# Optimization experiments

Measured on AMD Instinct MI355X. Metric: run time of the kernel, lower is better.

Reference implementation:

```python
import math
import jax, jax.numpy as jnp
import numpy as np

EMB = 1024
HEADS = 16
HEAD_DIM = EMB // HEADS
FF = 4 * EMB
EPS = 1e-5


def gelu_tanh(x):
    c = math.sqrt(2.0 / math.pi)
    return 0.5 * x * (1.0 + jnp.tanh(c * (x + 0.044715 * x ** 3)))


def layernorm(x, scale, shift):
    mean = jnp.mean(x, axis=-1, keepdims=True)
    var = jnp.var(x, axis=-1, keepdims=True)
    return scale * (x - mean) / jnp.sqrt(var + EPS) + shift


def setup_inputs() -> dict:
    key = jax.random.key(0)
    ks = jax.random.split(key, 10)
    s = 0.02
    return {
        "x": jax.random.normal(ks[0], (2, 2048, EMB), dtype=jnp.float32),
        "Wq": jax.random.normal(ks[1], (EMB, EMB), dtype=jnp.float32) * s,
        "Wk": jax.random.normal(ks[2], (EMB, EMB), dtype=jnp.float32) * s,
        "Wv": jax.random.normal(ks[3], (EMB, EMB), dtype=jnp.float32) * s,
        "Wo": jax.random.normal(ks[4], (EMB, EMB), dtype=jnp.float32) * s,
        "bo": jnp.zeros((EMB,), dtype=jnp.float32),
        "W1": jax.random.normal(ks[5], (EMB, FF), dtype=jnp.float32) * s,
        "b1": jnp.zeros((FF,), dtype=jnp.float32),
        "W2": jax.random.normal(ks[6], (FF, EMB), dtype=jnp.float32) * s,
        "b2": jnp.zeros((EMB,), dtype=jnp.float32),
        "ln1_scale": jnp.ones((EMB,), dtype=jnp.float32),
        "ln1_shift": jnp.zeros((EMB,), dtype=jnp.float32),
        "ln2_scale": jnp.ones((EMB,), dtype=jnp.float32),
        "ln2_shift": jnp.zeros((EMB,), dtype=jnp.float32),
    }


def reference(x, Wq, Wk, Wv, Wo, bo, W1, b1, W2, b2,
              ln1_scale, ln1_shift, ln2_scale, ln2_shift):
    B, S, D = x.shape
    # --- pre-LN causal MHA ---
    h = layernorm(x, ln1_scale, ln1_shift)
    q = (h @ Wq).reshape(B, S, HEADS, HEAD_DIM).transpose(0, 2, 1, 3)  # [B,H,S,d]
    k = (h @ Wk).reshape(B, S, HEADS, HEAD_DIM).transpose(0, 2, 1, 3)
    v = (h @ Wv).reshape(B, S, HEADS, HEAD_DIM).transpose(0, 2, 1, 3)
    scores = jnp.einsum("bhqd,bhkd->bhqk", q, k)  # [B,H,S,S]
    causal = jnp.triu(jnp.ones((S, S), dtype=bool), k=1)
    scores = jnp.where(causal, -jnp.inf, scores)
    attn = jax.nn.softmax(scores / math.sqrt(HEAD_DIM), axis=-1)
    ctx = jnp.einsum("bhqk,bhkd->bhqd", attn, v)  # [B,H,S,d]
    ctx = ctx.transpose(0, 2, 1, 3).reshape(B, S, D)
    x = x + (ctx @ Wo + bo)
    # --- FFN ---
    h = layernorm(x, ln2_scale, ln2_shift)
    h = gelu_tanh(h @ W1 + b1) @ W2 + b2
    return x + h
```

## Files before the change

### kernel.cpp

```cpp
#include <hip/hip_runtime.h>
#include <hip/hip_bf16.h>
#include <math.h>

#define EMB 1024
#define HEADS 16
#define HEAD_DIM 64
#define FF_DIM 4096
#define SEQ 2048
#define BATCH 2
#define NTOK (BATCH * SEQ)
#define LN_EPS 1e-5f
#define QKV_N 3072
#define Q_PRESCALE 0.18033688011112042f

typedef __attribute__((ext_vector_type(8))) short s8v;
typedef __attribute__((ext_vector_type(4))) float f4v;

__device__ __forceinline__ unsigned short f2bf(float f) {
    union { __hip_bfloat16 h; unsigned short u; } cv;
    cv.h = __float2bfloat16(f);
    return cv.u;
}

__device__ __forceinline__ float fast_exp2(float x) {
#if __has_builtin(__builtin_amdgcn_exp2f)
    return __builtin_amdgcn_exp2f(x);
#else
    return exp2f(x);
#endif
}

__device__ __forceinline__ float gelu_f(float x) {
    const float c = 0.7978845608028654f;
    float x3 = x * x * x;
    return 0.5f * x * (1.0f + tanhf(c * (x + 0.044715f * x3)));
}

#define GLDS(gp, lp)                                                        \
    __builtin_amdgcn_global_load_lds(                                       \
        (const __attribute__((address_space(1))) void*)(gp),                \
        (__attribute__((address_space(3))) void*)(lp), 16, 0, 0)

#define BAR()   do { __builtin_amdgcn_s_barrier(); __builtin_amdgcn_sched_barrier(0); } while (0)
#define LGKM0() do { asm volatile("s_waitcnt lgkmcnt(0)" ::: "memory"); __builtin_amdgcn_sched_barrier(0); } while (0)
#define VMCNT(n) do { asm volatile("s_waitcnt vmcnt(" #n ")" ::: "memory"); __builtin_amdgcn_sched_barrier(0); } while (0)

__global__ __launch_bounds__(256) void ln_bf16_kernel(const float* __restrict__ x,
                                                      const float* __restrict__ scale,
                                                      const float* __restrict__ shift,
                                                      unsigned short* __restrict__ out) {
    int row = blockIdx.x;
    int tid = threadIdx.x;
    const float4 xv = ((const float4*)(x + (size_t)row * EMB))[tid];
    float s  = xv.x + xv.y + xv.z + xv.w;
    float ss = xv.x * xv.x + xv.y * xv.y + xv.z * xv.z + xv.w * xv.w;
    __shared__ float2 red[256];
    red[tid] = make_float2(s, ss);
    __syncthreads();
    for (int off = 128; off > 0; off >>= 1) {
        if (tid < off) {
            red[tid].x += red[tid + off].x;
            red[tid].y += red[tid + off].y;
        }
        __syncthreads();
    }
    float mean = red[0].x * (1.0f / EMB);
    float var  = red[0].y * (1.0f / EMB) - mean * mean;
    float rstd = rsqrtf(var + LN_EPS);
    float4 sc4 = ((const float4*)scale)[tid];
    float4 sh4 = ((const float4*)shift)[tid];
    ushort4 o;
    o.x = f2bf(sc4.x * (xv.x - mean) * rstd + sh4.x);
    o.y = f2bf(sc4.y * (xv.y - mean) * rstd + sh4.y);
    o.z = f2bf(sc4.z * (xv.z - mean) * rstd + sh4.z);
    o.w = f2bf(sc4.w * (xv.w - mean) * rstd + sh4.w);
    *(ushort4*)(out + (size_t)row * EMB + tid * 4) = o;
}

__device__ __forceinline__ void tconv_tile(const float* __restrict__ W,
                                           unsigned short* __restrict__ Wt,
                                           int K, int N, int bx, int by, int tid) {
    __shared__ float t[64][65];
    int n0 = bx * 64, k0 = by * 64;
#pragma unroll
    for (int it = 0; it < 4; ++it) {
        int f = tid + it * 256;
        int r = f >> 4, c = (f & 15) * 4;
        float4 w = *(const float4*)(W + (size_t)(k0 + r) * N + n0 + c);
        t[r][c] = w.x; t[r][c + 1] = w.y; t[r][c + 2] = w.z; t[r][c + 3] = w.w;
    }
    __syncthreads();
#pragma unroll
    for (int it = 0; it < 4; ++it) {
        int f = tid + it * 256;
        int rn = f >> 4, ck = (f & 15) * 4;
        ushort4 o;
        o.x = f2bf(t[ck + 0][rn]);
        o.y = f2bf(t[ck + 1][rn]);
        o.z = f2bf(t[ck + 2][rn]);
        o.w = f2bf(t[ck + 3][rn]);
        *(ushort4*)(Wt + (size_t)(n0 + rn) * K + k0 + ck) = o;
    }
}

__global__ __launch_bounds__(256) void tconv_all_kernel(
    const float* __restrict__ Wq, const float* __restrict__ Wk,
    const float* __restrict__ Wv, const float* __restrict__ Wo,
    const float* __restrict__ W1, const float* __restrict__ W2,
    unsigned short* __restrict__ Wqkv_t, unsigned short* __restrict__ Wo_t,
    unsigned short* __restrict__ W1_t, unsigned short* __restrict__ W2_t) {
    int b = blockIdx.x;
    int tid = threadIdx.x;
    if (b < 256)        tconv_tile(Wq, Wqkv_t,                      EMB, EMB,    b & 15, b >> 4, tid);
    else if (b < 512)   tconv_tile(Wk, Wqkv_t + (size_t)1024 * EMB, EMB, EMB,    (b - 256) & 15, (b - 256) >> 4, tid);
    else if (b < 768)   tconv_tile(Wv, Wqkv_t + (size_t)2048 * EMB, EMB, EMB,    (b - 512) & 15, (b - 512) >> 4, tid);
    else if (b < 1024)  tconv_tile(Wo, Wo_t,                        EMB, EMB,    (b - 768) & 15, (b - 768) >> 4, tid);
    else if (b < 2048)  tconv_tile(W1, W1_t,                        EMB, FF_DIM, (b - 1024) & 63, (b - 1024) >> 6, tid);
    else                tconv_tile(W2, W2_t,                        FF_DIM, EMB, (b - 2048) & 15, (b - 2048) >> 4, tid);
}

__global__ __launch_bounds__(256) void reduce_kernel(const float* __restrict__ p0,
                                                     const float* __restrict__ p1,
                                                     const float* __restrict__ bias,
                                                     const float* __restrict__ residual,
                                                     float* __restrict__ out) {
    size_t i4 = ((size_t)blockIdx.x * 256 + threadIdx.x) * 4;
    float4 a = *(const float4*)(p0 + i4);
    float4 b = *(const float4*)(p1 + i4);
    float4 r = *(const float4*)(residual + i4);
    int col = (int)(i4 & (EMB - 1));
    float4 bs = *(const float4*)(bias + col);
    float4 o;
    o.x = a.x + b.x + r.x + bs.x;
    o.y = a.y + b.y + r.y + bs.y;
    o.z = a.z + b.z + r.z + bs.z;
    o.w = a.w + b.w + r.w + bs.w;
    *(float4*)(out + i4) = o;
}

__global__ __launch_bounds__(256) void reduce_ln_kernel(const float* __restrict__ p0,
                                                        const float* __restrict__ p1,
                                                        const float* __restrict__ bias,
                                                        const float* __restrict__ residual,
                                                        float* __restrict__ x1,
                                                        const float* __restrict__ scale,
                                                        const float* __restrict__ shift,
                                                        unsigned short* __restrict__ out) {
    int row = blockIdx.x;
    int tid = threadIdx.x;
    size_t i4 = (size_t)row * EMB + tid * 4;
    float4 a = *(const float4*)(p0 + i4);
    float4 b = *(const float4*)(p1 + i4);
    float4 r = *(const float4*)(residual + i4);
    float4 bs = *(const float4*)(bias + tid * 4);
    float4 xv;
    xv.x = a.x + b.x + r.x + bs.x;
    xv.y = a.y + b.y + r.y + bs.y;
    xv.z = a.z + b.z + r.z + bs.z;
    xv.w = a.w + b.w + r.w + bs.w;
    *(float4*)(x1 + i4) = xv;

    float s  = xv.x + xv.y + xv.z + xv.w;
    float ss = xv.x * xv.x + xv.y * xv.y + xv.z * xv.z + xv.w * xv.w;
    __shared__ float2 red[256];
    red[tid] = make_float2(s, ss);
    __syncthreads();
    for (int off = 128; off > 0; off >>= 1) {
        if (tid < off) {
            red[tid].x += red[tid + off].x;
            red[tid].y += red[tid + off].y;
        }
        __syncthreads();
    }
    float mean = red[0].x * (1.0f / EMB);
    float var  = red[0].y * (1.0f / EMB) - mean * mean;
    float rstd = rsqrtf(var + LN_EPS);
    float4 sc4 = ((const float4*)scale)[tid];
    float4 sh4 = ((const float4*)shift)[tid];
    ushort4 o;
    o.x = f2bf(sc4.x * (xv.x - mean) * rstd + sh4.x);
    o.y = f2bf(sc4.y * (xv.y - mean) * rstd + sh4.y);
    o.z = f2bf(sc4.z * (xv.z - mean) * rstd + sh4.z);
    o.w = f2bf(sc4.w * (xv.w - mean) * rstd + sh4.w);
    *(ushort4*)(out + i4) = o;
}

__global__ __launch_bounds__(512, 2) void gemm_8ph_kernel(
    const unsigned short* __restrict__ A,
    const unsigned short* __restrict__ Bt,
    unsigned short* __restrict__ Cb,
    int M, int N, int K,
    const float* __restrict__ bias,
    int do_gelu, int qkv_mode,
    unsigned short* __restrict__ vt)
{
    __shared__ short lds[65536];

    int tid = threadIdx.x;
    int w = tid >> 6, lane = tid & 63;
    int wr = w >> 2, wc = w & 3;
    int quad = lane >> 4, ln = lane & 15;

    int nbx = N >> 8;
    int nwg = (M >> 8) * nbx;
    int bid = (int)blockIdx.x;
    int swz = (nwg & 7) ? bid : ((bid & 7) * (nwg >> 3) + (bid >> 3));
    int by = swz / nbx, bx = swz - by * nbx;
    int m0 = by << 8, n0 = bx << 8;

    f4v acc[8][4];
#pragma unroll
    for (int i = 0; i < 8; ++i)
#pragma unroll
        for (int j = 0; j < 4; ++j) { f4v z = {0.f, 0.f, 0.f, 0.f}; acc[i][j] = z; }

    size_t Kby = (size_t)K << 1;
    size_t AhS = (size_t)128 * Kby;
    const char* AgC = (const char*)A + (size_t)(m0 + (tid & 127)) * Kby + (size_t)((tid >> 7) << 4);
    const char* BgC = (const char*)Bt + (size_t)(n0 + (tid & 127)) * Kby + (size_t)((tid >> 7) << 4);
    char* ldsC = (char*)lds;
    int tid16 = tid << 4;

    const short* aRd = lds + wr * 8192 + quad * 1024 + ln * 8;
    const short* bRd = lds + 32768 + (wc >> 1) * 8192 + (wc & 1) * 512 + quad * 1024 + ln * 8;

#define STG_A(tb, h, b) do {                                                     \
    const char* s_ = AgC + (size_t)(h) * AhS + (size_t)(tb);                     \
    char* d_ = ldsC + (b) * 32768 + (h) * 16384 + tid16;                         \
    GLDS(s_, d_); GLDS(s_ + 64, d_ + 8192); } while (0)
#define STG_B(tb, h, b) do {                                                     \
    const char* s_ = BgC + (size_t)(h) * AhS + (size_t)(tb);                     \
    char* d_ = ldsC + 65536 + (b) * 32768 + (h) * 16384 + tid16;                 \
    GLDS(s_, d_); GLDS(s_ + 64, d_ + 8192); } while (0)
#define RD_A4(mg, b) do {                                                        \
    _Pragma("unroll") for (int f_ = 0; f_ < 4; ++f_) {                           \
        af[f_][0] = *(const s8v*)(aRd + (b) * 16384 + ((mg) * 4 + f_) * 128);    \
        af[f_][1] = *(const s8v*)(aRd + (b) * 16384 + 4096 + ((mg) * 4 + f_) * 128); } } while (0)
#define RD_B2(dst, ng, b) do {                                                   \
    _Pragma("unroll") for (int g_ = 0; g_ < 2; ++g_) {                           \
        dst[g_][0] = *(const s8v*)(bRd + (b) * 16384 + ((ng) * 2 + g_) * 128);   \
        dst[g_][1] = *(const s8v*)(bRd + (b) * 16384 + 4096 + ((ng) * 2 + g_) * 128); } } while (0)
#define MF_Q(mg, bsrc, ng) do {                                                  \
    __builtin_amdgcn_s_setprio(1);                                               \
    _Pragma("unroll") for (int f_ = 0; f_ < 4; ++f_)                             \
    _Pragma("unroll") for (int g_ = 0; g_ < 2; ++g_)                             \
    _Pragma("unroll") for (int k_ = 0; k_ < 2; ++k_)                             \
        acc[(mg) * 4 + f_][(ng) * 2 + g_] = __builtin_amdgcn_mfma_f32_16x16x32_bf16( \
            af[f_][k_], bsrc[g_][k_], acc[(mg) * 4 + f_][(ng) * 2 + g_], 0, 0, 0); \
    __builtin_amdgcn_s_setprio(0); } while (0)

    s8v af[4][2], bf0[2][2], bf1[2][2];

    STG_A(0, 0, 0); STG_A(0, 1, 0);
    STG_B(0, 0, 0); STG_B(0, 1, 0);
    STG_B(128, 0, 1); STG_B(128, 1, 1);
    VMCNT(4);
    BAR();

    int nIter = K >> 7;
    for (int it = 0; it < nIter; ++it) {
        size_t base = (size_t)it << 8;
        bool pf = (it + 1 < nIter);

        RD_A4(0, 0); RD_B2(bf0, 0, 0);
        STG_A(base + 128, 0, 1);
        BAR(); LGKM0();
        MF_Q(0, bf0, 0);
        BAR();
        RD_B2(bf1, 1, 0);
        STG_A(base + 128, 1, 1);
        BAR(); LGKM0();
        MF_Q(0, bf1, 1);
        BAR();
        RD_A4(1, 0);
        if (pf) STG_B(base + 256, 0, 0);
        BAR(); LGKM0();
        MF_Q(1, bf0, 0);
        BAR();
        if (pf) STG_B(base + 256, 1, 0);
        BAR();
        MF_Q(1, bf1, 1);
        if (pf) { VMCNT(4); } else { VMCNT(0); }
        BAR();

        RD_A4(0, 1); RD_B2(bf0, 0, 1);
        if (pf) STG_A(base + 256, 0, 0);
        BAR(); LGKM0();
        MF_Q(0, bf0, 0);
        BAR();
        RD_B2(bf1, 1, 1);
        if (pf) STG_A(base + 256, 1, 0);
        BAR(); LGKM0();
        MF_Q(0, bf1, 1);
        BAR();
        RD_A4(1, 1);
        if (pf) STG_B(base + 384, 0, 1);
        BAR(); LGKM0();
        MF_Q(1, bf0, 0);
        BAR();
        if (pf) STG_B(base + 384, 1, 1);
        BAR();
        MF_Q(1, bf1, 1);
        if (pf) VMCNT(4);
        BAR();
    }
#undef STG_A
#undef STG_B
#undef RD_A4
#undef RD_B2
#undef MF_Q

    int cn  = n0 + wc * 64 + ln;
    int cm0 = m0 + wr * 128 + quad * 4;

    if (qkv_mode) {
        if (n0 < 2048) {
            float sc = (n0 < 1024) ? Q_PRESCALE : 1.0f;
#pragma unroll
            for (int g = 0; g < 4; ++g) {
                int gn = cn + g * 16;
#pragma unroll
                for (int f = 0; f < 8; ++f)
#pragma unroll
                    for (int r = 0; r < 4; ++r)
                        Cb[(size_t)(cm0 + f * 16 + r) * 2048 + gn] = f2bf(acc[f][g][r] * sc);
            }
        } else {
#pragma unroll
            for (int g = 0; g < 4; ++g) {
                int gn = cn + g * 16 - 2048;
#pragma unroll
                for (int f = 0; f < 8; ++f) {
                    int gm0 = cm0 + f * 16;
                    int bb = gm0 >> 11, s0 = gm0 & 2047;
                    ushort4 pk;
                    pk.x = f2bf(acc[f][g][0]);
                    pk.y = f2bf(acc[f][g][1]);
                    pk.z = f2bf(acc[f][g][2]);
                    pk.w = f2bf(acc[f][g][3]);
                    *(ushort4*)(vt + ((size_t)bb * 1024 + gn) * SEQ + s0) = pk;
                }
            }
        }
        return;
    }

#pragma unroll
    for (int g = 0; g < 4; ++g) {
        int gn = cn + g * 16;
        float bj = bias ? bias[gn] : 0.f;
#pragma unroll
        for (int f = 0; f < 8; ++f)
#pragma unroll
            for (int r = 0; r < 4; ++r) {
                float vv = acc[f][g][r] + bj;
                if (do_gelu) vv = gelu_f(vv);
                Cb[(size_t)(cm0 + f * 16 + r) * N + gn] = f2bf(vv);
            }
    }
}

__global__ __launch_bounds__(256) void gemm_bf16_kernel(
    const unsigned short* __restrict__ A,
    const unsigned short* __restrict__ Bt,
    float* __restrict__ Cf0,
    float* __restrict__ Cf1,
    int M, int N, int K, int Klen)
{
    __shared__ short As[2][4096];
    __shared__ short Bs[2][4096];

    int tid = threadIdx.x;
    int nbx = N >> 7, nby8 = (M >> 7) >> 3;
    int bid = (int)blockIdx.x;
    int xcd = bid & 7;
    int t   = bid >> 3;
    int x   = t % nbx;
    int u   = t / nbx;
    int y   = (u % nby8) * 8 + xcd;
    int z   = u / nby8;

    int m0 = y << 7;
    int n0 = x << 7;
    int k0 = z * Klen;
    float* Cf = z ? Cf1 : Cf0;
    int wv = tid >> 6, lane = tid & 63;
    int wr = wv >> 1, wc = wv & 1;
    int quad = lane >> 4, ln = lane & 15;

    f4v acc[4][4];
#pragma unroll
    for (int i = 0; i < 4; ++i)
#pragma unroll
        for (int j = 0; j < 4; ++j) {
            f4v z4 = {0.f, 0.f, 0.f, 0.f};
            acc[i][j] = z4;
        }

    int r0 = tid & 127;
    size_t Kby = (size_t)K << 1;
    const char* Ag0 = (const char*)A + (size_t)(m0 + r0) * Kby + (size_t)k0 * 2 + (tid >> 7) * 16;
    const char* Bg0 = (const char*)Bt + (size_t)(n0 + r0) * Kby + (size_t)k0 * 2 + (tid >> 7) * 16;

    int nIter = Klen >> 5;
    GLDS(Ag0, (char*)As[0] + tid * 16);
    GLDS(Ag0 + 32, (char*)As[0] + tid * 16 + 4096);
    GLDS(Bg0, (char*)Bs[0] + tid * 16);
    GLDS(Bg0 + 32, (char*)Bs[0] + tid * 16 + 4096);

    for (int it = 0; it < nIter; ++it) {
        VMCNT(0);
        BAR();
        if (it + 1 < nIter) {
            int kb = (it + 1) << 6;
            char* Ad = (char*)As[(it + 1) & 1] + tid * 16;
            char* Bd = (char*)Bs[(it + 1) & 1] + tid * 16;
            GLDS(Ag0 + kb, Ad);
            GLDS(Ag0 + kb + 32, Ad + 4096);
            GLDS(Bg0 + kb, Bd);
            GLDS(Bg0 + kb + 32, Bd + 4096);
            __builtin_amdgcn_sched_barrier(0);
        }
        const short* Ab = As[it & 1];
        const short* Bb = Bs[it & 1];
        s8v af[4], bfr[4];
#pragma unroll
        for (int i = 0; i < 4; ++i)
            af[i] = *(const s8v*)(Ab + ((size_t)quad * 128 + wr * 64 + i * 16 + ln) * 8);
#pragma unroll
        for (int j = 0; j < 4; ++j)
            bfr[j] = *(const s8v*)(Bb + ((size_t)quad * 128 + wc * 64 + j * 16 + ln) * 8);
#pragma unroll
        for (int i = 0; i < 4; ++i)
#pragma unroll
            for (int j = 0; j < 4; ++j)
                acc[i][j] = __builtin_amdgcn_mfma_f32_16x16x32_bf16(af[i], bfr[j], acc[i][j], 0, 0, 0);
    }

    int cn  = n0 + wc * 64 + ln;
    int cm0 = m0 + wr * 64 + quad * 4;
#pragma unroll
    for (int j = 0; j < 4; ++j) {
        int gn = cn + j * 16;
#pragma unroll
        for (int i = 0; i < 4; ++i)
#pragma unroll
            for (int r = 0; r < 4; ++r)
                Cf[(size_t)(cm0 + i * 16 + r) * N + gn] = acc[i][j][r];
    }
}

__global__ __launch_bounds__(256) void flash_attn_mfma_kernel(
    const unsigned short* __restrict__ qk,
    const unsigned short* __restrict__ vt,
    unsigned short* __restrict__ ctx)
{
    int h  = blockIdx.x;
    int b  = blockIdx.z;
    int qt = b ? (int)blockIdx.y : ((int)gridDim.y - 1 - (int)blockIdx.y);
    int tid = threadIdx.x;
    int w = tid >> 6, lane = tid & 63;
    int quad = lane >> 4, ln = lane & 15;

    __shared__ short Kb2[2][4096];
    __shared__ short Vb2[2][4096];
    __shared__ short Ps[4][32 * 72];

    size_t qrow0 = (size_t)b * SEQ + (size_t)qt * 128;
    int wrow0 = w * 32;

    s8v qf[2][2];
#pragma unroll
    for (int mb = 0; mb < 2; ++mb)
#pragma unroll
        for (int ks = 0; ks < 2; ++ks)
            qf[mb][ks] = *(const s8v*)(qk + (qrow0 + wrow0 + mb * 16 + ln) * 2048
                                          + h * 64 + ks * 32 + quad * 8);

    float l_part[2][4];
    f4v o[2][4];
#pragma unroll
    for (int mb = 0; mb < 2; ++mb) {
#pragma unroll
        for (int r = 0; r < 4; ++r) l_part[mb][r] = 0.f;
#pragma unroll
        for (int db = 0; db < 4; ++db) {
            f4v z = {0.f, 0.f, 0.f, 0.f};
            o[mb][db] = z;
        }
    }

    const unsigned short* kb_p = qk + (size_t)b * SEQ * 2048 + 1024 + h * 64;
    const unsigned short* vb_p = vt + ((size_t)b * 1024 + h * 64) * SEQ;
    short* Pw = Ps[w];

    int rr = tid & 63;
    const unsigned short* Kg0 = kb_p + (size_t)rr * 2048 + (tid >> 6) * 8;
    const unsigned short* Vg0 = vb_p + (size_t)rr * 2048 + (tid >> 6) * 8;

    int ktn = 2 * qt + 2;
    int ktmax_w = (qt * 128 + wrow0 + 31) >> 6;

    GLDS(Kg0, (char*)Kb2[0] + tid * 16);
    GLDS(Kg0 + 32, (char*)Kb2[0] + tid * 16 + 4096);
    GLDS(Vg0, (char*)Vb2[0] + tid * 16);
    GLDS(Vg0 + 32, (char*)Vb2[0] + tid * 16 + 4096);

    for (int kt = 0; kt < ktn; ++kt) {
        BAR();
        bool pf = (kt + 1 < ktn);
        if (pf) {
            int nb_ = (kt + 1) & 1;
            const unsigned short* ks_ = Kg0 + (size_t)(kt + 1) * 64 * 2048;
            const unsigned short* vs_ = Vg0 + (kt + 1) * 64;
            GLDS(ks_, (char*)Kb2[nb_] + tid * 16);
            GLDS(ks_ + 32, (char*)Kb2[nb_] + tid * 16 + 4096);
            GLDS(vs_, (char*)Vb2[nb_] + tid * 16);
            GLDS(vs_ + 32, (char*)Vb2[nb_] + tid * 16 + 4096);
        }
        if (kt > ktmax_w) continue;
        if (pf) { VMCNT(8); } else { VMCNT(0); }

        const short* Kl = Kb2[kt & 1];
        const short* Vl = Vb2[kt & 1];

        f4v s[2][4];
#pragma unroll
        for (int mb = 0; mb < 2; ++mb)
#pragma unroll
            for (int nb = 0; nb < 4; ++nb) {
                f4v z = {0.f, 0.f, 0.f, 0.f};
                s[mb][nb] = z;
            }
#pragma unroll
        for (int ks = 0; ks < 2; ++ks)
#pragma unroll
            for (int nb = 0; nb < 4; ++nb) {
                s8v kfr = *(const s8v*)(Kl + ((size_t)(ks * 4 + quad) * 64 + nb * 16 + ln) * 8);
#pragma unroll
                for (int mb = 0; mb < 2; ++mb)
                    s[mb][nb] = __builtin_amdgcn_mfma_f32_16x16x32_bf16(qf[mb][ks], kfr, s[mb][nb], 0, 0, 0);
            }

        bool edge = (kt == ktmax_w);
#pragma unroll
        for (int mb = 0; mb < 2; ++mb) {
#pragma unroll
            for (int r = 0; r < 4; ++r) {
                int rloc = mb * 16 + quad * 4 + r;
                float p[4];
                if (!edge) {
#pragma unroll
                    for (int nb = 0; nb < 4; ++nb)
                        p[nb] = fast_exp2(s[mb][nb][r]);
                } else {
                    int grow = qt * 128 + wrow0 + rloc;
#pragma unroll
                    for (int nb = 0; nb < 4; ++nb) {
                        int key = kt * 64 + nb * 16 + ln;
                        float e = fast_exp2(s[mb][nb][r]);
                        p[nb] = (key > grow) ? 0.f : e;
                    }
                }
                l_part[mb][r] += (p[0] + p[1]) + (p[2] + p[3]);
#pragma unroll
                for (int nb = 0; nb < 4; ++nb)
                    Pw[rloc * 72 + nb * 16 + ln] = f2bf(p[nb]);
            }
        }

#pragma unroll
        for (int ks = 0; ks < 2; ++ks) {
            s8v pf_[2];
#pragma unroll
            for (int mb = 0; mb < 2; ++mb)
                pf_[mb] = *(const s8v*)(Pw + (mb * 16 + ln) * 72 + ks * 32 + quad * 8);
#pragma unroll
            for (int db = 0; db < 4; ++db) {
                s8v vfr = *(const s8v*)(Vl + ((size_t)(ks * 4 + quad) * 64 + db * 16 + ln) * 8);
#pragma unroll
                for (int mb = 0; mb < 2; ++mb)
                    o[mb][db] = __builtin_amdgcn_mfma_f32_16x16x32_bf16(pf_[mb], vfr, o[mb][db], 0, 0, 0);
            }
        }
    }

    asm volatile("s_waitcnt vmcnt(0)" ::: "memory");

#pragma unroll
    for (int mb = 0; mb < 2; ++mb)
#pragma unroll
        for (int r = 0; r < 4; ++r) {
            float l = l_part[mb][r];
#pragma unroll
            for (int msk = 1; msk < 16; msk <<= 1)
                l += __shfl_xor(l, msk);
            float inv = 1.0f / l;
            size_t row = qrow0 + wrow0 + mb * 16 + quad * 4 + r;
#pragma unroll
            for (int db = 0; db < 4; ++db)
                ctx[row * EMB + h * 64 + db * 16 + ln] = f2bf(o[mb][db][r] * inv);
        }
}

extern "C" void kernel_launch(void* const* d_in, const int* in_sizes, int n_in,
                              void* d_out, int out_size, void* d_ws, size_t ws_size,
                              hipStream_t stream) {
    const float* x    = (const float*)d_in[0];
    const float* Wq   = (const float*)d_in[1];
    const float* Wk   = (const float*)d_in[2];
    const float* Wv   = (const float*)d_in[3];
    const float* Wo   = (const float*)d_in[4];
    const float* bo   = (const float*)d_in[5];
    const float* W1   = (const float*)d_in[6];
    const float* b1   = (const float*)d_in[7];
    const float* W2   = (const float*)d_in[8];
    const float* b2   = (const float*)d_in[9];
    const float* ln1s = (const float*)d_in[10];
    const float* ln1b = (const float*)d_in[11];
    const float* ln2s = (const float*)d_in[12];
    const float* ln2b = (const float*)d_in[13];
    float* out = (float*)d_out;

    const size_t MiB = 1024 * 1024;
    uint8_t* w8 = (uint8_t*)d_ws;
    unsigned short* Wqkv_t = (unsigned short*)(w8);
    unsigned short* Wo_t   = (unsigned short*)(w8 +  6 * MiB);
    unsigned short* W1_t   = (unsigned short*)(w8 +  8 * MiB);
    unsigned short* W2_t   = (unsigned short*)(w8 + 16 * MiB);
    unsigned short* act_bf = (unsigned short*)(w8 + 24 * MiB);
    unsigned short* qk_bf  = (unsigned short*)(w8 + 32 * MiB);
    unsigned short* vt     = (unsigned short*)(w8 + 48 * MiB);
    float*          p0a    = (float*)(w8 + 32 * MiB);
    float*          p1a    = (float*)(w8 + 48 * MiB);
    unsigned short* u_bf   = (unsigned short*)(w8 + 32 * MiB);
    float*          x1     = (float*)(w8 + 64 * MiB);
    float*          p0b    = (float*)(w8);
    float*          p1b    = (float*)(w8 + 80 * MiB);

    tconv_all_kernel<<<3072, 256, 0, stream>>>(Wq, Wk, Wv, Wo, W1, W2,
                                               Wqkv_t, Wo_t, W1_t, W2_t);

    ln_bf16_kernel<<<NTOK, 256, 0, stream>>>(x, ln1s, ln1b, act_bf);

    gemm_8ph_kernel<<<(NTOK / 256) * (QKV_N / 256), 512, 0, stream>>>(
        act_bf, Wqkv_t, qk_bf, NTOK, QKV_N, EMB, nullptr, 0, 1, vt);

    flash_attn_mfma_kernel<<<dim3(HEADS, SEQ / 128, BATCH), 256, 0, stream>>>(qk_bf, vt, act_bf);

    gemm_bf16_kernel<<<(EMB / 128) * (NTOK / 128) * 2, 256, 0, stream>>>(
        act_bf, Wo_t, p0a, p1a, NTOK, EMB, EMB, 512);
    reduce_ln_kernel<<<NTOK, 256, 0, stream>>>(p0a, p1a, bo, x, x1, ln2s, ln2b, act_bf);

    gemm_8ph_kernel<<<(NTOK / 256) * (FF_DIM / 256), 512, 0, stream>>>(
        act_bf, W1_t, u_bf, NTOK, FF_DIM, EMB, b1, 1, 0, nullptr);

    gemm_bf16_kernel<<<(EMB / 128) * (NTOK / 128) * 2, 256, 0, stream>>>(
        u_bf, W2_t, p0b, p1b, NTOK, EMB, FF_DIM, 2048);
    reduce_kernel<<<(NTOK * EMB) / 1024, 256, 0, stream>>>(p0b, p1b, b2, x1, out);
}
```

Before: 426.3 us.

## Stage GEMM epilogues through LDS for coalesced stores and double K-step depth

```diff
diff --git a/kernel.cpp b/kernel.cpp
--- a/kernel.cpp
+++ b/kernel.cpp
@@ -310,53 +310,63 @@
 #undef RD_B2
 #undef MF_Q
 
-    int cn  = n0 + wc * 64 + ln;
-    int cm0 = m0 + wr * 128 + quad * 4;
-
-    if (qkv_mode) {
-        if (n0 < 2048) {
-            float sc = (n0 < 1024) ? Q_PRESCALE : 1.0f;
-#pragma unroll
-            for (int g = 0; g < 4; ++g) {
-                int gn = cn + g * 16;
-#pragma unroll
-                for (int f = 0; f < 8; ++f)
-#pragma unroll
-                    for (int r = 0; r < 4; ++r)
-                        Cb[(size_t)(cm0 + f * 16 + r) * 2048 + gn] = f2bf(acc[f][g][r] * sc);
+    int colb = wc * 64 + ln;
+    int rowb = wr * 128 + quad * 4;
+    int off8 = (tid & 31) * 8;
+    int sub  = tid >> 5;
+
+    if (qkv_mode && n0 >= 2048) {
+#pragma unroll
+        for (int g = 0; g < 4; ++g) {
+            int c = colb + g * 16;
+            int swz = (c & 7) << 3;
+#pragma unroll
+            for (int f = 0; f < 8; ++f) {
+                int rw = rowb + f * 16;
+                ushort4 pk;
+                pk.x = f2bf(acc[f][g][0]);
+                pk.y = f2bf(acc[f][g][1]);
+                pk.z = f2bf(acc[f][g][2]);
+                pk.w = f2bf(acc[f][g][3]);
+                *(ushort4*)(lds + c * 256 + (rw ^ swz)) = pk;
             }
-        } else {
-#pragma unroll
-            for (int g = 0; g < 4; ++g) {
-                int gn = cn + g * 16 - 2048;
-#pragma unroll
-                for (int f = 0; f < 8; ++f) {
-                    int gm0 = cm0 + f * 16;
-                    int bb = gm0 >> 11, s0 = gm0 & 2047;
-                    ushort4 pk;
-                    pk.x = f2bf(acc[f][g][0]);
-                    pk.y = f2bf(acc[f][g][1]);
-                    pk.z = f2bf(acc[f][g][2]);
-                    pk.w = f2bf(acc[f][g][3]);
-                    *(ushort4*)(vt + ((size_t)bb * 1024 + gn) * SEQ + s0) = pk;
-                }
+        }
+        BAR();
+        int bb = m0 >> 11, s0b = m0 & 2047;
+        size_t vbase = ((size_t)bb * 1024 + (n0 - 2048)) * SEQ + s0b + off8;
+#pragma unroll
+        for (int pass = 0; pass < 16; ++pass) {
+            int c = pass * 16 + sub;
+            s8v v = *(const s8v*)(lds + c * 256 + (off8 ^ ((c & 7) << 3)));
+            *(s8v*)(vt + vbase + (size_t)c * SEQ) = v;
+        }
+        return;
+    }
+
+    bool isq = qkv_mode && (n0 < 1024);
+#pragma unroll
+    for (int g = 0; g < 4; ++g) {
+        int c = colb + g * 16;
+        float bj = (!qkv_mode && bias) ? bias[n0 + c] : 0.f;
+#pragma unroll
+        for (int f = 0; f < 8; ++f) {
+            int rw = rowb + f * 16;
+#pragma unroll
+            for (int r = 0; r < 4; ++r) {
+                float vv = acc[f][g][r];
+                if (qkv_mode) { if (isq) vv *= Q_PRESCALE; }
+                else { vv += bj; if (do_gelu) vv = gelu_f(vv); }
+                lds[(rw + r) * 256 + c] = (short)f2bf(vv);
             }
         }
-        return;
-    }
-
-#pragma unroll
-    for (int g = 0; g < 4; ++g) {
-        int gn = cn + g * 16;
-        float bj = bias ? bias[gn] : 0.f;
-#pragma unroll
-        for (int f = 0; f < 8; ++f)
-#pragma unroll
-            for (int r = 0; r < 4; ++r) {
-                float vv = acc[f][g][r] + bj;
-                if (do_gelu) vv = gelu_f(vv);
-                Cb[(size_t)(cm0 + f * 16 + r) * N + gn] = f2bf(vv);
-            }
+    }
+    BAR();
+    int ldc = qkv_mode ? 2048 : N;
+#pragma unroll
+    for (int pass = 0; pass < 16; ++pass) {
+        int rw = pass * 16 + sub;
+        s8v v = *(const s8v*)(lds + rw * 256 + off8);
+        *(s8v*)(Cb + (size_t)(m0 + rw) * ldc + n0 + off8) = v;
     }
 }
 
@@ -367,8 +377,8 @@
     float* __restrict__ Cf1,
     int M, int N, int K, int Klen)
 {
-    __shared__ short As[2][4096];
-    __shared__ short Bs[2][4096];
+    __shared__ short As[2][8192];
+    __shared__ short Bs[2][8192];
 
     int tid = threadIdx.x;
     int nbx = N >> 7, nby8 = (M >> 7) >> 3;
@@ -402,39 +412,47 @@
     const char* Ag0 = (const char*)A + (size_t)(m0 + r0) * Kby + (size_t)k0 * 2 + (tid >> 7) * 16;
     const char* Bg0 = (const char*)Bt + (size_t)(n0 + r0) * Kby + (size_t)k0 * 2 + (tid >> 7) * 16;
 
-    int nIter = Klen >> 5;
-    GLDS(Ag0, (char*)As[0] + tid * 16);
-    GLDS(Ag0 + 32, (char*)As[0] + tid * 16 + 4096);
-    GLDS(Bg0, (char*)Bs[0] + tid * 16);
-    GLDS(Bg0 + 32, (char*)Bs[0] + tid * 16 + 4096);
+    int nIter = Klen >> 6;
+#pragma unroll
+    for (int p = 0; p < 4; ++p) {
+        GLDS(Ag0 + p * 32, (char*)As[0] + p * 4096 + tid * 16);
+        GLDS(Bg0 + p * 32, (char*)Bs[0] + p * 4096 + tid * 16);
+    }
 
     for (int it = 0; it < nIter; ++it) {
         VMCNT(0);
         BAR();
         if (it + 1 < nIter) {
-            int kb = (it + 1) << 6;
-            char* Ad = (char*)As[(it + 1) & 1] + tid * 16;
-            char* Bd = (char*)Bs[(it + 1) & 1] + tid * 16;
-            GLDS(Ag0 + kb, Ad);
-            GLDS(Ag0 + kb + 32, Ad + 4096);
-            GLDS(Bg0 + kb, Bd);
-            GLDS(Bg0 + kb + 32, Bd + 4096);
+            int kb = (it + 1) << 7;
+            char* Ad = (char*)As[(it + 1) & 1];
+            char* Bd = (char*)Bs[(it + 1) & 1];
+#pragma unroll
+            for (int p = 0; p < 4; ++p) {
+                GLDS(Ag0 + kb + p * 32, Ad + p * 4096 + tid * 16);
+                GLDS(Bg0 + kb + p * 32, Bd + p * 4096 + tid * 16);
+            }
             __builtin_amdgcn_sched_barrier(0);
         }
         const short* Ab = As[it & 1];
         const short* Bb = Bs[it & 1];
-        s8v af[4], bfr[4];
-#pragma unroll
-        for (int i = 0; i < 4; ++i)
-            af[i] = *(const s8v*)(Ab + ((size_t)quad * 128 + wr * 64 + i * 16 + ln) * 8);
-#pragma unroll
-        for (int j = 0; j < 4; ++j)
-            bfr[j] = *(const s8v*)(Bb + ((size_t)quad * 128 + wc * 64 + j * 16 + ln) * 8);
-#pragma unroll
-        for (int i = 0; i < 4; ++i)
+        s8v af[2][4], bfr[2][4];
+#pragma unroll
+        for (int ks = 0; ks < 2; ++ks)
+#pragma unroll
+            for (int i = 0; i < 4; ++i)
+                af[ks][i] = *(const s8v*)(Ab + ((size_t)(ks * 4 + quad) * 128 + wr * 64 + i * 16 + ln) * 8);
+#pragma unroll
+        for (int ks = 0; ks < 2; ++ks)
 #pragma unroll
             for (int j = 0; j < 4; ++j)
-                acc[i][j] = __builtin_amdgcn_mfma_f32_16x16x32_bf16(af[i], bfr[j], acc[i][j], 0, 0, 0);
+                bfr[ks][j] = *(const s8v*)(Bb + ((size_t)(ks * 4 + quad) * 128 + wc * 64 + j * 16 + ln) * 8);
+#pragma unroll
+        for (int ks = 0; ks < 2; ++ks)
+#pragma unroll
+            for (int i = 0; i < 4; ++i)
+#pragma unroll
+                for (int j = 0; j < 4; ++j)
+                    acc[i][j] = __builtin_amdgcn_mfma_f32_16x16x32_bf16(af[ks][i], bfr[ks][j], acc[i][j], 0, 0, 0);
     }
 
     int cn  = n0 + wc * 64 + ln;
```

After: 435.9 us. 2.3% more time.
